# Performance work log

Measured on AMD Instinct MI355X. Metric: run time of the kernel, lower is better.

## Reference

```python
import jax, jax.numpy as jnp
import numpy as np

ANCHORS = np.array([[10.,13.],[16.,30.],[33.,23.],[30.,61.],[62.,45.],
                    [59.,119.],[116.,90.],[156.,198.],[373.,326.]], dtype=np.float32)
ANCHOR_MASK = [[6,7,8],[3,4,5],[0,1,2]]
INPUT_WH = np.array([320., 320.], dtype=np.float32)  # (W, H) == input_shape[::-1] (square)
IGNORE_THRESH = 0.5
NUM_CLASSES = 80
GRIDS = [10, 20, 40]
BATCH = 4


def _bce_logits(labels, logits):
    # tf.nn.sigmoid_cross_entropy_with_logits
    return jnp.maximum(logits, 0.0) - logits * labels + jnp.log1p(jnp.exp(-jnp.abs(logits)))


def _yolo_head(feats, anchors):
    gh, gw = feats.shape[1], feats.shape[2]
    gx = jnp.arange(gw, dtype=feats.dtype)
    gy = jnp.arange(gh, dtype=feats.dtype)
    # grid[..., 0] = x, grid[..., 1] = y ; shape [gh, gw, 1, 2]
    grid = jnp.stack(jnp.meshgrid(gx, gy), axis=-1)[:, :, None, :]
    box_xy = (jax.nn.sigmoid(feats[..., :2]) + grid) / jnp.array([gw, gh], feats.dtype)
    anc = jnp.asarray(anchors, feats.dtype).reshape(1, 1, 1, -1, 2)
    box_wh = jnp.exp(feats[..., 2:4]) * anc / jnp.asarray(INPUT_WH, feats.dtype)
    return grid, box_xy, box_wh


def _pairwise_iou(p, t):
    # p: [B,P,4] pred boxes (cx,cy,w,h); t: [B,N,4] true boxes -> iou [B,P,N]
    p_min = p[:, :, None, :2] - p[:, :, None, 2:4] * 0.5
    p_max = p[:, :, None, :2] + p[:, :, None, 2:4] * 0.5
    t_min = t[:, None, :, :2] - t[:, None, :, 2:4] * 0.5
    t_max = t[:, None, :, :2] + t[:, None, :, 2:4] * 0.5
    wh = jnp.maximum(jnp.minimum(p_max, t_max) - jnp.maximum(p_min, t_min), 0.0)
    inter = wh[..., 0] * wh[..., 1]
    p_area = p[:, :, None, 2] * p[:, :, None, 3]
    t_area = t[:, None, :, 2] * t[:, None, :, 3]
    return inter / (p_area + t_area - inter)


def _layer_loss(t, y, anchors, g):
    obj = t[..., 4:5]                      # [B,g,g,3,1]
    objb = obj != 0
    grid, pxy, pwh = _yolo_head(y, anchors)
    pred_box = jnp.concatenate([pxy, pwh], axis=-1)
    raw_true_xy = t[..., :2] * jnp.array([g, g], t.dtype) - grid
    anc = jnp.asarray(anchors, t.dtype).reshape(1, 1, 1, -1, 2)
    wh_scaled = t[..., 2:4] * jnp.asarray(INPUT_WH, t.dtype) / anc
    raw_true_wh = jnp.where(objb, jnp.log(jnp.where(objb, wh_scaled, 1.0)), 0.0)
    box_scale = 2.0 - t[..., 2:3] * t[..., 3:4]

    # ignore mask: masked pairwise IoU (all-slots, statically shaped; mask = objectness)
    B = t.shape[0]
    P = g * g * 3
    pb = pred_box.reshape(B, P, 4)
    tb = t[..., :4].reshape(B, P, 4)
    tmask = (t[..., 4] != 0).reshape(B, P)
    iou = _pairwise_iou(pb, tb)                         # [B,P,P]
    iou = jnp.where(tmask[:, None, :], iou, -jnp.inf)
    best_iou = jnp.max(iou, axis=-1)                    # -inf when no true boxes (matches empty reduce_max)
    ignore = (best_iou < IGNORE_THRESH).astype(t.dtype).reshape(obj.shape)

    xy_loss = obj * box_scale * _bce_logits(raw_true_xy, y[..., 0:2])
    wh_loss = obj * box_scale * 0.5 * jnp.square(raw_true_wh - y[..., 2:4])
    conf_loss = (obj + (1.0 - obj) * ignore) * _bce_logits(obj, y[..., 4:5])
    cls_loss = obj * _bce_logits(t[..., 5:], y[..., 5:])

    per_img = (xy_loss.sum((1, 2, 3, 4)) + wh_loss.sum((1, 2, 3, 4))
               + conf_loss.sum((1, 2, 3, 4)) + cls_loss.sum((1, 2, 3, 4)))
    return jnp.mean(per_img)


def setup_inputs() -> dict:
    key = jax.random.key(0)
    inp = {}
    for l, g in enumerate(GRIDS):
        k = jax.random.fold_in(key, l)
        k1, k2, k3, k4, k5 = jax.random.split(k, 5)
        xy = jax.random.uniform(k1, (BATCH, g, g, 3, 2), jnp.float32)
        wh = jax.random.uniform(k2, (BATCH, g, g, 3, 2), jnp.float32, 0.05, 0.9)
        obj = jax.random.bernoulli(k3, 0.02, (BATCH, g, g, 3, 1)).astype(jnp.float32)
        cls = jax.random.uniform(k4, (BATCH, g, g, 3, NUM_CLASSES), jnp.float32)
        inp[f"t{l}"] = jnp.concatenate([xy, wh, obj, cls], axis=-1)
        inp[f"y{l}"] = jax.random.normal(k5, (BATCH, g, g, 3, 5 + NUM_CLASSES), jnp.float32)
    return inp


def reference(t0, t1, t2, y0, y1, y2):
    targets = [t0, t1, t2]
    outputs = [y0, y1, y2]
    loss = jnp.float32(0.0)
    for l in range(3):
        loss = loss + _layer_loss(targets[l], outputs[l], ANCHORS[ANCHOR_MASK[l]], GRIDS[l])
    return loss
```

## Files before the change

kernel.cpp:

```cpp
#include <hip/hip_runtime.h>
#include <math.h>

#define NBLK 104
#define SCAP 512

__device__ __constant__ float c_anc[3][3][2] = {
  {{116.f, 90.f}, {156.f, 198.f}, {373.f, 326.f}},
  {{ 30.f, 61.f}, { 62.f,  45.f}, { 59.f, 119.f}},
  {{ 10.f, 13.f}, { 16.f,  30.f}, { 33.f,  23.f}}};

__device__ __forceinline__ float bce_f(float label, float logit) {
    return fmaxf(logit, 0.0f) - logit * label + log1pf(expf(-fabsf(logit)));
}

template<int P, int G>
__device__ __forceinline__ float layer_block(
    const float* __restrict__ t, const float* __restrict__ y,
    int img, int chunk, const float (*anc)[2],
    float4* sbox, int* scount)
{
    const float* tslab = t + (size_t)img * P * 85;
    const float* yslab = y + (size_t)img * P * 85;

    if (threadIdx.x == 0) *scount = 0;
    __syncthreads();
    #pragma unroll 4
    for (int k = threadIdx.x; k < P; k += 256) {
        float obj = tslab[(size_t)k * 85 + 4];
        if (obj != 0.0f) {
            int off = atomicAdd(scount, 1);
            if (off < SCAP) {
                const float* tp = tslab + (size_t)k * 85;
                sbox[off] = make_float4(tp[0], tp[1], tp[2], tp[3]);
            }
        }
    }
    __syncthreads();
    int cnt = *scount; if (cnt > SCAP) cnt = SCAP;
    int cntPad = (cnt + 7) & ~7;
    for (int k = cnt + threadIdx.x; k < cntPad; k += 256)
        sbox[k] = make_float4(0.f, 0.f, 0.f, 0.f);
    __syncthreads();

    int pos = chunk * 256 + threadIdx.x;
    bool valid = pos < P;
    float acc = 0.0f, obj = 0.0f;
    if (valid) {
        const float* yp = yslab + (size_t)pos * 85;
        obj = tslab[(size_t)pos * 85 + 4];
        float q0 = yp[0], q1 = yp[1], q2 = yp[2], q3 = yp[3], q4 = yp[4];
        int a = pos % 3, cell = pos / 3;
        int j = cell % G, i = cell / G;
        float aw = anc[a][0], ah = anc[a][1];
        float gi = (float)G;

        float px = (1.0f / (1.0f + expf(-q0)) + (float)j) / gi;
        float py = (1.0f / (1.0f + expf(-q1)) + (float)i) / gi;
        float pw = expf(q2) * aw * (1.0f / 320.0f);
        float ph = expf(q3) * ah * (1.0f / 320.0f);
        float phx = pw * 0.5f, phy = ph * 0.5f;
        float pminx = px - phx, pmaxx = px + phx;
        float pminy = py - phy, pmaxy = py + phy;
        float parea = pw * ph;

        float best = -INFINITY;
        for (int k0 = 0; k0 < cntPad; k0 += 8) {
            #pragma unroll
            for (int u = 0; u < 8; ++u) {
                float4 tb = sbox[k0 + u];
                float thx = tb.z * 0.5f, thy = tb.w * 0.5f;
                float wx = fminf(pmaxx, tb.x + thx) - fmaxf(pminx, tb.x - thx);
                float wy = fminf(pmaxy, tb.y + thy) - fmaxf(pminy, tb.y - thy);
                wx = fmaxf(wx, 0.0f);
                wy = fmaxf(wy, 0.0f);
                float inter = wx * wy;
                float iou = inter / (parea + tb.z * tb.w - inter);
                best = fmaxf(best, iou);
            }
        }
        float ignore = (best < 0.5f) ? 1.0f : 0.0f;
        float bce_c = fmaxf(q4, 0.0f) - q4 * obj + log1pf(expf(-fabsf(q4)));
        acc = (obj + (1.0f - obj) * ignore) * bce_c;
    }

    unsigned long long m = __ballot(valid && obj != 0.0f);
    int lane = threadIdx.x & 63;
    int waveBase = chunk * 256 + (threadIdx.x & ~63);
    while (m) {
        int b = __ffsll(m) - 1; m &= m - 1;
        int ppos = waveBase + b;
        const float* tp = tslab + (size_t)ppos * 85;
        const float* yp = yslab + (size_t)ppos * 85;
        float tv1 = tp[lane], yv1 = yp[lane];
        bool has2 = lane < 21;
        float tv2 = 0.f, yv2 = 0.f;
        if (has2) { tv2 = tp[lane + 64]; yv2 = yp[lane + 64]; }

        float tw = __shfl(tv1, 2, 64);
        float th = __shfl(tv1, 3, 64);
        float bs = 2.0f - tw * th;
        int a = ppos % 3, cell = ppos / 3;
        int jj = cell % G, ii = cell / G;
        float aw = anc[a][0], ah = anc[a][1];

        float term;
        if (lane == 0)      term = bs * bce_f(tv1 * (float)G - (float)jj, yv1);
        else if (lane == 1) term = bs * bce_f(tv1 * (float)G - (float)ii, yv1);
        else if (lane == 2) { float d = logf(tv1 * 320.0f / aw) - yv1; term = bs * 0.5f * d * d; }
        else if (lane == 3) { float d = logf(tv1 * 320.0f / ah) - yv1; term = bs * 0.5f * d * d; }
        else if (lane == 4) term = 0.0f;
        else                term = bce_f(tv1, yv1);
        if (has2) term += bce_f(tv2, yv2);
        acc += term;
    }
    return acc;
}

__global__ __launch_bounds__(256) void k_all(
    const float* __restrict__ t0, const float* __restrict__ y0,
    const float* __restrict__ t1, const float* __restrict__ y1,
    const float* __restrict__ t2, const float* __restrict__ y2,
    float* __restrict__ partials)
{
    __shared__ float4 sbox[SCAP];
    __shared__ int scount;
    int blk = blockIdx.x;

    float acc;
    if (blk < 8)       acc = layer_block< 300, 10>(t0, y0, blk >> 1, blk & 1,  c_anc[0], sbox, &scount);
    else if (blk < 28) { int r = blk - 8;  acc = layer_block<1200, 20>(t1, y1, r / 5,  r % 5,  c_anc[1], sbox, &scount); }
    else               { int r = blk - 28; acc = layer_block<4800, 40>(t2, y2, r / 19, r % 19, c_anc[2], sbox, &scount); }

    float v = acc;
    #pragma unroll
    for (int o = 32; o > 0; o >>= 1) v += __shfl_down(v, o, 64);
    __shared__ float red[4];
    int lane = threadIdx.x & 63, w = threadIdx.x >> 6;
    if (lane == 0) red[w] = v;
    __syncthreads();
    if (threadIdx.x == 0)
        partials[blk] = ((red[0] + red[1]) + (red[2] + red[3])) * 0.25f;
}

__global__ __launch_bounds__(128) void k_fin(
    const float* __restrict__ partials, float* __restrict__ out)
{
    int tid = threadIdx.x;
    float s = (tid < NBLK) ? partials[tid] : 0.0f;
    #pragma unroll
    for (int o = 32; o > 0; o >>= 1) s += __shfl_down(s, o, 64);
    __shared__ float r2[2];
    if ((tid & 63) == 0) r2[tid >> 6] = s;
    __syncthreads();
    if (tid == 0) out[0] = r2[0] + r2[1];
}

extern "C" void kernel_launch(void* const* d_in, const int* in_sizes, int n_in,
                              void* d_out, int out_size, void* d_ws, size_t ws_size,
                              hipStream_t stream) {
    const float* t0 = (const float*)d_in[0];
    const float* y0 = (const float*)d_in[1];
    const float* t1 = (const float*)d_in[2];
    const float* y1 = (const float*)d_in[3];
    const float* t2 = (const float*)d_in[4];
    const float* y2 = (const float*)d_in[5];

    float* partials = (float*)d_ws;
    float* out      = (float*)d_out;

    k_all<<<NBLK, 256, 0, stream>>>(t0, y0, t1, y1, t2, y2, partials);
    k_fin<<<1, 128, 0, stream>>>(partials, out);
}
```

Measured before the change: 33.90 us.

## Add wide pre-scan kernel to compact objectness, boxes and logits; fuse final reduction

Adds a 2048-block scan kernel that streams t and y with coalesced float4 loads. It writes a compact objectness flag array, the boxes of object cells, and the first five logit channels per anchor slot into workspace. The main kernel then reads these compact buffers instead of 85-float-strided rows, which is meant to cut uncoalesced gather traffic in the 104-block kernel. The separate finalize kernel is replaced by a last-block-done atomic reduction. In exchange the scan reads the full t and y tensors once more with a much wider grid and adds an extra launch, and the done counter depends on being reset by the scan kernel.

```diff
diff --git a/kernel.cpp b/kernel.cpp
--- a/kernel.cpp
+++ b/kernel.cpp
@@ -1,8 +1,10 @@
 #include <hip/hip_runtime.h>
 #include <math.h>
 
+
 #define NBLK 104
 #define SCAP 512
+#define NT4 535500
 
 __device__ __constant__ float c_anc[3][3][2] = {
   {{116.f, 90.f}, {156.f, 198.f}, {373.f, 326.f}},
@@ -13,25 +15,69 @@
     return fmaxf(logit, 0.0f) - logit * label + log1pf(expf(-fabsf(logit)));
 }
 
+__global__ __launch_bounds__(256) void k_scan(
+    const float* __restrict__ t0, const float* __restrict__ y0,
+    const float* __restrict__ t1, const float* __restrict__ y1,
+    const float* __restrict__ t2, const float* __restrict__ y2,
+    float* __restrict__ flag, float4* __restrict__ boxes,
+    float* __restrict__ qbuf, int* __restrict__ done)
+{
+    int gid = blockIdx.x * 256 + threadIdx.x;
+    if (gid == 0) *done = 0;
+    int stride = gridDim.x * 256;
+    for (int i = gid; i < 2 * NT4; i += stride) {
+        bool isY = i >= NT4;
+        int f4 = isY ? i - NT4 : i;
+        const float* src; int rowBase, fi;
+        if (f4 < 25500)       { src = isY ? y0 : t0; fi = f4 * 4;              rowBase = 0;    }
+        else if (f4 < 127500) { src = isY ? y1 : t1; fi = (f4 - 25500) * 4;    rowBase = 1200; }
+        else                  { src = isY ? y2 : t2; fi = (f4 - 127500) * 4;   rowBase = 6000; }
+        float4 v = *(const float4*)(src + fi);
+        float xs[4] = {v.x, v.y, v.z, v.w};
+        #pragma unroll
+        for (int c = 0; c < 4; ++c) {
+            int f = fi + c;
+            int row = f / 85;
+            int ch  = f - row * 85;
+            float x = xs[c];
+            int grow = rowBase + row;
+            if (!isY) {
+                if (ch == 4) {
+                    flag[grow] = x;
+                    if (x != 0.0f) {
+                        const float* tp = src + (size_t)row * 85;
+                        boxes[grow] = make_float4(tp[0], tp[1], tp[2], tp[3]);
+                    }
+                }
+            } else {
+                if (ch < 5) qbuf[grow * 5 + ch] = x;
+            }
+        }
+    }
+}
+
 template<int P, int G>
 __device__ __forceinline__ float layer_block(
     const float* __restrict__ t, const float* __restrict__ y,
-    int img, int chunk, const float (*anc)[2],
+    int img, int chunk, int rowBase, const float (*anc)[2],
+    const float* __restrict__ flag, const float4* __restrict__ boxes,
+    const float* __restrict__ qbuf,
     float4* sbox, int* scount)
 {
-    const float* tslab = t + (size_t)img * P * 85;
-    const float* yslab = y + (size_t)img * P * 85;
+    const int gbase = rowBase + img * P;
+    const float* fimg = flag + gbase;
 
     if (threadIdx.x == 0) *scount = 0;
     __syncthreads();
-    #pragma unroll 4
-    for (int k = threadIdx.x; k < P; k += 256) {
-        float obj = tslab[(size_t)k * 85 + 4];
-        if (obj != 0.0f) {
-            int off = atomicAdd(scount, 1);
-            if (off < SCAP) {
-                const float* tp = tslab + (size_t)k * 85;
-                sbox[off] = make_float4(tp[0], tp[1], tp[2], tp[3]);
+    const float4* fimg4 = (const float4*)fimg;
+    for (int k4 = threadIdx.x; k4 < P / 4; k4 += 256) {
+        float4 fv = fimg4[k4];
+        float fs[4] = {fv.x, fv.y, fv.z, fv.w};
+        #pragma unroll
+        for (int c = 0; c < 4; ++c) {
+            if (fs[c] != 0.0f) {
+                int off = atomicAdd(scount, 1);
+                if (off < SCAP) sbox[off] = boxes[gbase + k4 * 4 + c];
             }
         }
     }
@@ -46,9 +92,9 @@
     bool valid = pos < P;
     float acc = 0.0f, obj = 0.0f;
     if (valid) {
-        const float* yp = yslab + (size_t)pos * 85;
-        obj = tslab[(size_t)pos * 85 + 4];
-        float q0 = yp[0], q1 = yp[1], q2 = yp[2], q3 = yp[3], q4 = yp[4];
+        const float* qp = qbuf + (size_t)(gbase + pos) * 5;
+        float q0 = qp[0], q1 = qp[1], q2 = qp[2], q3 = qp[3], q4 = qp[4];
+        obj = fimg[pos];
         int a = pos % 3, cell = pos / 3;
         int j = cell % G, i = cell / G;
         float aw = anc[a][0], ah = anc[a][1];
@@ -83,6 +129,8 @@
         acc = (obj + (1.0f - obj) * ignore) * bce_c;
     }
 
+    const float* tslab = t + (size_t)img * P * 85;
+    const float* yslab = y + (size_t)img * P * 85;
     unsigned long long m = __ballot(valid && obj != 0.0f);
     int lane = threadIdx.x & 63;
     int waveBase = chunk * 256 + (threadIdx.x & ~63);
@@ -116,20 +164,23 @@
     return acc;
 }
 
-__global__ __launch_bounds__(256) void k_all(
+__global__ __launch_bounds__(256) void k_main(
     const float* __restrict__ t0, const float* __restrict__ y0,
     const float* __restrict__ t1, const float* __restrict__ y1,
     const float* __restrict__ t2, const float* __restrict__ y2,
-    float* __restrict__ partials)
+    const float* __restrict__ flag, const float4* __restrict__ boxes,
+    const float* __restrict__ qbuf,
+    float* __restrict__ partials, int* __restrict__ done,
+    float* __restrict__ out)
 {
     __shared__ float4 sbox[SCAP];
     __shared__ int scount;
     int blk = blockIdx.x;
 
     float acc;
-    if (blk < 8)       acc = layer_block< 300, 10>(t0, y0, blk >> 1, blk & 1,  c_anc[0], sbox, &scount);
-    else if (blk < 28) { int r = blk - 8;  acc = layer_block<1200, 20>(t1, y1, r / 5,  r % 5,  c_anc[1], sbox, &scount); }
-    else               { int r = blk - 28; acc = layer_block<4800, 40>(t2, y2, r / 19, r % 19, c_anc[2], sbox, &scount); }
+    if (blk < 8)       acc = layer_block< 300, 10>(t0, y0, blk >> 1, blk & 1, 0, c_anc[0], flag, boxes, qbuf, sbox, &scount);
+    else if (blk < 28) { int r = blk - 8;  acc = layer_block<1200, 20>(t1, y1, r / 5,  r % 5,  1200, c_anc[1], flag, boxes, qbuf, sbox, &scount); }
+    else               { int r = blk - 28; acc = layer_block<4800, 40>(t2, y2, r / 19, r % 19, 6000, c_anc[2], flag, boxes, qbuf, sbox, &scount); }
 
     float v = acc;
     #pragma unroll
@@ -138,21 +189,25 @@
     int lane = threadIdx.x & 63, w = threadIdx.x >> 6;
     if (lane == 0) red[w] = v;
     __syncthreads();
-    if (threadIdx.x == 0)
-        partials[blk] = ((red[0] + red[1]) + (red[2] + red[3])) * 0.25f;
-}
-
-__global__ __launch_bounds__(128) void k_fin(
-    const float* __restrict__ partials, float* __restrict__ out)
-{
-    int tid = threadIdx.x;
-    float s = (tid < NBLK) ? partials[tid] : 0.0f;
-    #pragma unroll
-    for (int o = 32; o > 0; o >>= 1) s += __shfl_down(s, o, 64);
-    __shared__ float r2[2];
-    if ((tid & 63) == 0) r2[tid >> 6] = s;
-    __syncthreads();
-    if (tid == 0) out[0] = r2[0] + r2[1];
+
+    if (threadIdx.x < 64) {
+        int old = 0;
+        if (threadIdx.x == 0) {
+            float p = ((red[0] + red[1]) + (red[2] + red[3])) * 0.25f;
+            __hip_atomic_store(&partials[blk], p, __ATOMIC_RELAXED, __HIP_MEMORY_SCOPE_AGENT);
+            old = __hip_atomic_fetch_add(done, 1, __ATOMIC_ACQ_REL, __HIP_MEMORY_SCOPE_AGENT);
+        }
+        old = __shfl(old, 0, 64);
+        if (old == NBLK - 1) {
+            float s = 0.0f;
+            if (lane < NBLK - 64)
+                s = __hip_atomic_load(&partials[lane + 64], __ATOMIC_RELAXED, __HIP_MEMORY_SCOPE_AGENT);
+            s += __hip_atomic_load(&partials[lane], __ATOMIC_RELAXED, __HIP_MEMORY_SCOPE_AGENT);
+            #pragma unroll
+            for (int o = 32; o > 0; o >>= 1) s += __shfl_down(s, o, 64);
+            if (lane == 0) out[0] = s;
+        }
+    }
 }
 
 extern "C" void kernel_launch(void* const* d_in, const int* in_sizes, int n_in,
@@ -165,9 +220,13 @@
     const float* t2 = (const float*)d_in[4];
     const float* y2 = (const float*)d_in[5];
 
-    float* partials = (float*)d_ws;
-    float* out      = (float*)d_out;
-
-    k_all<<<NBLK, 256, 0, stream>>>(t0, y0, t1, y1, t2, y2, partials);
-    k_fin<<<1, 128, 0, stream>>>(partials, out);
-}
+    float*  flag     = (float*)d_ws;
+    float4* boxes    = (float4*)((char*)d_ws + 102400);
+    float*  qbuf     = (float*)((char*)d_ws + 512000);
+    float*  partials = (float*)((char*)d_ws + 1016064);
+    int*    done     = (int*)((char*)d_ws + 1020160);
+    float*  out      = (float*)d_out;
+
+    k_scan<<<2048, 256, 0, stream>>>(t0, y0, t1, y1, t2, y2, flag, boxes, qbuf, done);
+    k_main<<<NBLK, 256, 0, stream>>>(t0, y0, t1, y1, t2, y2, flag, boxes, qbuf, partials, done, out);
+}
```

Result: no change. 34.57 us (+2.0%).

## Use 1024-thread blocks, prefetch predictions, and fuse final reduction via last-block atomic

Applied to the files above, without the earlier changes.

Each block now has 1024 threads instead of 256, which cuts the grid from 104 to 32 blocks, so each image slab's true-box compaction runs fewer times overall. Each thread's prediction and objectness values are loaded before the compaction barrier so that global load latency overlaps with the scan. The separate finalize kernel is replaced by an agent-scope atomic counter, and the last block to finish sums the partials. A tiny init kernel that zeroes the counter is still launched, so the launch count is unchanged. Using fewer, larger blocks leaves much of the GPU idle and raises register pressure per block.

```diff
diff --git a/kernel.cpp b/kernel.cpp
--- a/kernel.cpp
+++ b/kernel.cpp
@@ -1,7 +1,7 @@
 #include <hip/hip_runtime.h>
 #include <math.h>
 
-#define NBLK 104
+#define NBLK 32
 #define SCAP 512
 
 __device__ __constant__ float c_anc[3][3][2] = {
@@ -13,6 +13,10 @@
     return fmaxf(logit, 0.0f) - logit * label + log1pf(expf(-fabsf(logit)));
 }
 
+__global__ void k_init(int* __restrict__ done) {
+    if (threadIdx.x == 0) *done = 0;
+}
+
 template<int P, int G>
 __device__ __forceinline__ float layer_block(
     const float* __restrict__ t, const float* __restrict__ y,
@@ -21,13 +25,21 @@
 {
     const float* tslab = t + (size_t)img * P * 85;
     const float* yslab = y + (size_t)img * P * 85;
+    const int tid = threadIdx.x;
 
-    if (threadIdx.x == 0) *scount = 0;
+    int pos = chunk * 1024 + tid;
+    bool valid = pos < P;
+    int ppre = valid ? pos : 0;
+    const float* qp = yslab + (size_t)ppre * 85;
+    float q0 = qp[0], q1 = qp[1], q2 = qp[2], q3 = qp[3], q4 = qp[4];
+    float obj = tslab[(size_t)ppre * 85 + 4];
+    if (!valid) obj = 0.0f;
+
+    if (tid == 0) *scount = 0;
     __syncthreads();
-    #pragma unroll 4
-    for (int k = threadIdx.x; k < P; k += 256) {
-        float obj = tslab[(size_t)k * 85 + 4];
-        if (obj != 0.0f) {
+    for (int k = tid; k < P; k += 1024) {
+        float o = tslab[(size_t)k * 85 + 4];
+        if (o != 0.0f) {
             int off = atomicAdd(scount, 1);
             if (off < SCAP) {
                 const float* tp = tslab + (size_t)k * 85;
@@ -38,17 +50,12 @@
     __syncthreads();
     int cnt = *scount; if (cnt > SCAP) cnt = SCAP;
     int cntPad = (cnt + 7) & ~7;
-    for (int k = cnt + threadIdx.x; k < cntPad; k += 256)
+    for (int k = cnt + tid; k < cntPad; k += 1024)
         sbox[k] = make_float4(0.f, 0.f, 0.f, 0.f);
     __syncthreads();
 
-    int pos = chunk * 256 + threadIdx.x;
-    bool valid = pos < P;
-    float acc = 0.0f, obj = 0.0f;
+    float acc = 0.0f;
     if (valid) {
-        const float* yp = yslab + (size_t)pos * 85;
-        obj = tslab[(size_t)pos * 85 + 4];
-        float q0 = yp[0], q1 = yp[1], q2 = yp[2], q3 = yp[3], q4 = yp[4];
         int a = pos % 3, cell = pos / 3;
         int j = cell % G, i = cell / G;
         float aw = anc[a][0], ah = anc[a][1];
@@ -84,8 +91,8 @@
     }
 
     unsigned long long m = __ballot(valid && obj != 0.0f);
-    int lane = threadIdx.x & 63;
-    int waveBase = chunk * 256 + (threadIdx.x & ~63);
+    int lane = tid & 63;
+    int waveBase = chunk * 1024 + (tid & ~63);
     while (m) {
         int b = __ffsll(m) - 1; m &= m - 1;
         int ppos = waveBase + b;
@@ -116,43 +123,49 @@
     return acc;
 }
 
-__global__ __launch_bounds__(256) void k_all(
+__global__ __launch_bounds__(1024) void k_all(
     const float* __restrict__ t0, const float* __restrict__ y0,
     const float* __restrict__ t1, const float* __restrict__ y1,
     const float* __restrict__ t2, const float* __restrict__ y2,
-    float* __restrict__ partials)
+    float* __restrict__ partials, int* __restrict__ done,
+    float* __restrict__ out)
 {
     __shared__ float4 sbox[SCAP];
     __shared__ int scount;
     int blk = blockIdx.x;
 
     float acc;
-    if (blk < 8)       acc = layer_block< 300, 10>(t0, y0, blk >> 1, blk & 1,  c_anc[0], sbox, &scount);
-    else if (blk < 28) { int r = blk - 8;  acc = layer_block<1200, 20>(t1, y1, r / 5,  r % 5,  c_anc[1], sbox, &scount); }
-    else               { int r = blk - 28; acc = layer_block<4800, 40>(t2, y2, r / 19, r % 19, c_anc[2], sbox, &scount); }
+    if (blk < 4)       acc = layer_block< 300, 10>(t0, y0, blk, 0, c_anc[0], sbox, &scount);
+    else if (blk < 12) { int r = blk - 4;  acc = layer_block<1200, 20>(t1, y1, r >> 1, r & 1, c_anc[1], sbox, &scount); }
+    else               { int r = blk - 12; acc = layer_block<4800, 40>(t2, y2, r / 5,  r % 5, c_anc[2], sbox, &scount); }
 
     float v = acc;
     #pragma unroll
     for (int o = 32; o > 0; o >>= 1) v += __shfl_down(v, o, 64);
-    __shared__ float red[4];
+    __shared__ float red[16];
     int lane = threadIdx.x & 63, w = threadIdx.x >> 6;
     if (lane == 0) red[w] = v;
     __syncthreads();
-    if (threadIdx.x == 0)
-        partials[blk] = ((red[0] + red[1]) + (red[2] + red[3])) * 0.25f;
-}
 
-__global__ __launch_bounds__(128) void k_fin(
-    const float* __restrict__ partials, float* __restrict__ out)
-{
-    int tid = threadIdx.x;
-    float s = (tid < NBLK) ? partials[tid] : 0.0f;
-    #pragma unroll
-    for (int o = 32; o > 0; o >>= 1) s += __shfl_down(s, o, 64);
-    __shared__ float r2[2];
-    if ((tid & 63) == 0) r2[tid >> 6] = s;
-    __syncthreads();
-    if (tid == 0) out[0] = r2[0] + r2[1];
+    if (threadIdx.x < 64) {
+        int old = 0;
+        if (threadIdx.x == 0) {
+            float s = 0.0f;
+            #pragma unroll
+            for (int q = 0; q < 16; ++q) s += red[q];
+            __hip_atomic_store(&partials[blk], s * 0.25f, __ATOMIC_RELAXED, __HIP_MEMORY_SCOPE_AGENT);
+            old = __hip_atomic_fetch_add(done, 1, __ATOMIC_ACQ_REL, __HIP_MEMORY_SCOPE_AGENT);
+        }
+        old = __shfl(old, 0, 64);
+        if (old == NBLK - 1) {
+            float s = 0.0f;
+            if (lane < NBLK)
+                s = __hip_atomic_load(&partials[lane], __ATOMIC_RELAXED, __HIP_MEMORY_SCOPE_AGENT);
+            #pragma unroll
+            for (int o = 32; o > 0; o >>= 1) s += __shfl_down(s, o, 64);
+            if (lane == 0) out[0] = s;
+        }
+    }
 }
 
 extern "C" void kernel_launch(void* const* d_in, const int* in_sizes, int n_in,
@@ -165,9 +178,10 @@
     const float* t2 = (const float*)d_in[4];
     const float* y2 = (const float*)d_in[5];
 
-    float* partials = (float*)d_ws;
+    int*   done     = (int*)d_ws;
+    float* partials = (float*)((char*)d_ws + 64);
     float* out      = (float*)d_out;
 
-    k_all<<<NBLK, 256, 0, stream>>>(t0, y0, t1, y1, t2, y2, partials);
-    k_fin<<<1, 128, 0, stream>>>(partials, out);
+    k_init<<<1, 64, 0, stream>>>(done);
+    k_all<<<NBLK, 1024, 0, stream>>>(t0, y0, t1, y1, t2, y2, partials, done, out);
 }
```

After: 43.89 us. 1.29x slower.
